# Performance work log

Hardware: AMD Instinct MI355X
Metric: run time of the kernel (lower is better)

## Reference

```python
import jax, jax.numpy as jnp
import numpy as np

T, B, IN_DIM, MEM_DIM = 512, 64, 512, 512


def _kaiming(key, shape):
    fan_in = shape[1]
    return jax.random.normal(key, shape, dtype=jnp.float32) * np.sqrt(2.0 / fan_in)


def setup_inputs() -> dict:
    key = jax.random.key(0)
    ks = jax.random.split(key, 5)
    return {
        "inputs": jax.random.normal(ks[0], (T, B, IN_DIM), dtype=jnp.float32),
        "h0": jnp.zeros((B, MEM_DIM), dtype=jnp.float32),
        "c0": jnp.zeros((B, MEM_DIM), dtype=jnp.float32),
        "W_ioux": _kaiming(ks[1], (3 * MEM_DIM, IN_DIM)),
        "b_ioux": jnp.zeros((3 * MEM_DIM,), dtype=jnp.float32),
        "W_iouh": _kaiming(ks[2], (3 * MEM_DIM, MEM_DIM)),
        "b_iouh": jnp.zeros((3 * MEM_DIM,), dtype=jnp.float32),
        "W_fx": _kaiming(ks[3], (MEM_DIM, IN_DIM)),
        "b_fx": jnp.zeros((MEM_DIM,), dtype=jnp.float32),
        "W_fh": _kaiming(ks[4], (MEM_DIM, MEM_DIM)),
        "b_fh": jnp.zeros((MEM_DIM,), dtype=jnp.float32),
    }


def reference(inputs, h0, c0, W_ioux, b_ioux, W_iouh, b_iouh, W_fx, b_fx, W_fh, b_fh):
    # Precompute input-side projections for all timesteps (one big GEMM each).
    x_iou = jnp.einsum('tbi,gi->tbg', inputs, W_ioux) + b_ioux  # [T,B,3M]
    x_f = jnp.einsum('tbi,mi->tbm', inputs, W_fx) + b_fx        # [T,B,M]

    def step(carry, xt):
        c, h = carry
        xiou_t, xf_t = xt
        iou = xiou_t + h @ W_iouh.T + b_iouh
        i, o, u = jnp.split(iou, 3, axis=-1)
        i = jax.nn.sigmoid(i)
        o = jax.nn.sigmoid(o)
        u = jnp.tanh(u)
        f = jax.nn.sigmoid(xf_t + h @ W_fh.T + b_fh)
        c_new = i * u + f * c
        h_new = o * jnp.tanh(c_new)
        return (c_new, h_new), h_new

    (c_final, h_final), output = jax.lax.scan(step, (c0, h0), (x_iou, x_f))
    # Matches torch: (stacked hidden states [T,B,M], final (c, h))
    return output, c_final, h_final
```

## Files before the change

kernel.cpp:

```cpp
#include <hip/hip_runtime.h>
#include <math.h>

#define T_STEPS 512
#define BATCH   64
#define INDIM   512
#define MEMDIM  512
#define NWG     256
#define NT      1024


#define SMEM_FLOATS (8*1028 + 4*8*68 + 16*8*68 + 2*64 + 8)

extern "C" __global__ void __launch_bounds__(NT, 1)
lstm_scan(const float* __restrict__ inputs, const float* __restrict__ h0,
          const float* __restrict__ c0,
          const float* __restrict__ W_ioux, const float* __restrict__ b_ioux,
          const float* __restrict__ W_iouh, const float* __restrict__ b_iouh,
          const float* __restrict__ W_fx,   const float* __restrict__ b_fx,
          const float* __restrict__ W_fh,   const float* __restrict__ b_fh,
          float* __restrict__ out, int* __restrict__ bar)
{
    extern __shared__ float smem[];
    float* W_s    = smem;
    float* xpart  = smem + 8*1028;
    float* hpart  = xpart + 4*8*68;
    float* c_s    = hpart + 16*8*68;
    float* bias_s = c_s + 2*64;

    float* hist = (float*)(bar + 2048);

    const int tid  = threadIdx.x;
    const int wg   = blockIdx.x;
    const int lane = tid & 63;
    const int wv16 = tid >> 6;

    const int q    = tid >> 8;
    const int r    = tid & 255;
    const int j8   = r & 7;
    const int bsub = (r >> 3) & 7;
    const int wv   = r >> 6;
    const int b0   = 16 * wv + bsub;
    const int b1   = b0 + 8;

    const int s    = lane & 31;
    const int dsub = lane >> 5;

    for (int i = tid; i < 8 * 256; i += NT) {
        int row = i >> 8;
        int c4  = i & 255;
        int mloc = row >> 2, gate = row & 3;
        int mg = 2 * wg + mloc;
        const float* src;
        if (c4 < 128) {
            const float* Wx = (gate < 3) ? (W_ioux + (size_t)(gate * 512 + mg) * INDIM)
                                         : (W_fx   + (size_t)mg * INDIM);
            src = Wx + c4 * 4;
        } else {
            const float* Wh = (gate < 3) ? (W_iouh + (size_t)(gate * 512 + mg) * MEMDIM)
                                         : (W_fh   + (size_t)mg * MEMDIM);
            src = Wh + (c4 - 128) * 4;
        }
        float4 v = *(const float4*)src;
        *(float4*)&W_s[row * 1028 + c4 * 4] = v;
    }
    if (tid < 8) {
        int mloc = tid >> 2, gate = tid & 3, mg = 2 * wg + mloc;
        bias_s[tid] = (gate < 3) ? (b_ioux[gate * 512 + mg] + b_iouh[gate * 512 + mg])
                                 : (b_fx[mg] + b_fh[mg]);
    }
    if (tid < 128) {
        int mloc = tid >> 6, b = tid & 63;
        c_s[mloc * 64 + b] = c0[(size_t)b * MEMDIM + 2 * wg + mloc];
        float hv = h0[(size_t)b * MEMDIM + 2 * wg + mloc];
        __hip_atomic_store(&hist[(2 * wg + mloc) * 64 + b], hv,
                           __ATOMIC_RELAXED, __HIP_MEMORY_SCOPE_AGENT);
    }
    __syncthreads();

    int* myflag = bar + 576 + (wg >> 4) * 32;
    if (tid == 0) {
        int n = __hip_atomic_fetch_add(&bar[(wg >> 4) * 32], 1, __ATOMIC_RELAXED,
                                       __HIP_MEMORY_SCOPE_AGENT);
        if (n == 15) {
            int m = __hip_atomic_fetch_add(&bar[512], 1, __ATOMIC_RELAXED,
                                           __HIP_MEMORY_SCOPE_AGENT);
            if (m == 15) {
                for (int l = 0; l < 16; ++l)
                    __hip_atomic_store(&bar[576 + l * 32], 1, __ATOMIC_RELAXED,
                                       __HIP_MEMORY_SCOPE_AGENT);
            }
        }
    }

    const float4* wrowx = (const float4*)&W_s[j8 * 1028] + q * 32;

    for (int t = 0; t < T_STEPS; ++t) {
        const float4* x0p = (const float4*)(inputs + ((size_t)t * BATCH + b0) * INDIM) + q * 32;
        const float4* x1p = (const float4*)(inputs + ((size_t)t * BATCH + b1) * INDIM) + q * 32;
        float4 a0 = make_float4(0.f, 0.f, 0.f, 0.f);
        float4 a1 = make_float4(0.f, 0.f, 0.f, 0.f);
#pragma unroll 8
        for (int k = 0; k < 32; ++k) {
            float4 w  = wrowx[k];
            float4 v0 = x0p[k];
            float4 v1 = x1p[k];
            a0.x += v0.x * w.x; a0.y += v0.y * w.y; a0.z += v0.z * w.z; a0.w += v0.w * w.w;
            a1.x += v1.x * w.x; a1.y += v1.y * w.y; a1.z += v1.z * w.z; a1.w += v1.w * w.w;
        }
        xpart[q * 544 + j8 * 68 + b0] = a0.x + a0.y + a0.z + a0.w;
        xpart[q * 544 + j8 * 68 + b1] = a1.x + a1.y + a1.z + a1.w;

        if (tid == 0) {
            while (__hip_atomic_load(myflag, __ATOMIC_RELAXED,
                                     __HIP_MEMORY_SCOPE_AGENT) < t + 1) {
                __builtin_amdgcn_s_sleep(1);
            }
        }
        __syncthreads();

        const unsigned long long* hrow =
            (const unsigned long long*)(hist + (size_t)(t & 1) * 32768);
        float2 hacc[8];
#pragma unroll
        for (int j = 0; j < 8; ++j) { hacc[j].x = 0.f; hacc[j].y = 0.f; }
#pragma unroll 4
        for (int it = 0; it < 16; ++it) {
            int d = wv16 * 32 + it * 2 + dsub;
            unsigned long long u = __hip_atomic_load(hrow + d * 32 + s,
                                                     __ATOMIC_RELAXED,
                                                     __HIP_MEMORY_SCOPE_AGENT);
            float2 hv = __builtin_bit_cast(float2, u);
#pragma unroll
            for (int j = 0; j < 8; ++j) {
                float wj = W_s[j * 1028 + 512 + d];
                hacc[j].x += wj * hv.x;
                hacc[j].y += wj * hv.y;
            }
        }
#pragma unroll
        for (int j = 0; j < 8; ++j) {
            hacc[j].x += __shfl_xor(hacc[j].x, 32);
            hacc[j].y += __shfl_xor(hacc[j].y, 32);
        }
        if (lane < 32) {
#pragma unroll
            for (int j = 0; j < 8; ++j)
                *(float2*)&hpart[wv16 * 544 + j * 68 + 2 * s] = hacc[j];
        }
        __syncthreads();

        float hn = 0.f, cn = 0.f;
        int mloc = tid >> 6, b = tid & 63;
        if (tid < 128) {
            float g[4];
#pragma unroll
            for (int gi = 0; gi < 4; ++gi) {
                int j = mloc * 4 + gi;
                float v = bias_s[j];
#pragma unroll
                for (int qq = 0; qq < 4; ++qq) v += xpart[qq * 544 + j * 68 + b];
#pragma unroll
                for (int w = 0; w < 16; ++w)  v += hpart[w * 544 + j * 68 + b];
                g[gi] = v;
            }
            float ig = 1.f / (1.f + expf(-g[0]));
            float og = 1.f / (1.f + expf(-g[1]));
            float ug = tanhf(g[2]);
            float fg = 1.f / (1.f + expf(-g[3]));
            cn = ig * ug + fg * c_s[mloc * 64 + b];
            c_s[mloc * 64 + b] = cn;
            hn = og * tanhf(cn);
            __hip_atomic_store(&hist[(size_t)((t + 1) & 1) * 32768
                                     + (2 * wg + mloc) * 64 + b], hn,
                               __ATOMIC_RELAXED, __HIP_MEMORY_SCOPE_AGENT);
        }
        __syncthreads();

        if (tid == 0) {
            int g16 = wg >> 4;
            int n = __hip_atomic_fetch_add(&bar[g16 * 32], 1, __ATOMIC_RELAXED,
                                           __HIP_MEMORY_SCOPE_AGENT);
            if (n == 16 * (t + 2) - 1) {
                int m = __hip_atomic_fetch_add(&bar[512], 1, __ATOMIC_RELAXED,
                                               __HIP_MEMORY_SCOPE_AGENT);
                if (m == 16 * (t + 2) - 1) {
                    for (int l = 0; l < 16; ++l)
                        __hip_atomic_store(&bar[576 + l * 32], t + 2,
                                           __ATOMIC_RELAXED, __HIP_MEMORY_SCOPE_AGENT);
                }
            }
        }

        if (tid < 128) {
            int mg = 2 * wg + mloc;
            out[((size_t)t * BATCH + b) * MEMDIM + mg] = hn;
            if (t == T_STEPS - 1) {
                out[(size_t)T_STEPS * BATCH * MEMDIM + (size_t)b * MEMDIM + mg] = cn;
                out[(size_t)T_STEPS * BATCH * MEMDIM + (size_t)BATCH * MEMDIM
                    + (size_t)b * MEMDIM + mg] = hn;
            }
        }
    }
}

extern "C" void kernel_launch(void* const* d_in, const int* in_sizes, int n_in,
                              void* d_out, int out_size, void* d_ws, size_t ws_size,
                              hipStream_t stream) {
    (void)in_sizes; (void)n_in; (void)out_size; (void)ws_size;
    const float* inputs = (const float*)d_in[0];
    const float* h0     = (const float*)d_in[1];
    const float* c0     = (const float*)d_in[2];
    const float* W_ioux = (const float*)d_in[3];
    const float* b_ioux = (const float*)d_in[4];
    const float* W_iouh = (const float*)d_in[5];
    const float* b_iouh = (const float*)d_in[6];
    const float* W_fx   = (const float*)d_in[7];
    const float* b_fx   = (const float*)d_in[8];
    const float* W_fh   = (const float*)d_in[9];
    const float* b_fh   = (const float*)d_in[10];
    float* out = (float*)d_out;
    int*   bar = (int*)d_ws;

    const size_t smem_bytes = SMEM_FLOATS * sizeof(float);
    (void)hipFuncSetAttribute((const void*)lstm_scan,
                              hipFuncAttributeMaxDynamicSharedMemorySize,
                              (int)smem_bytes);

    (void)hipMemsetAsync(d_ws, 0, 8192, stream);

    void* args[] = { (void*)&inputs, (void*)&h0, (void*)&c0,
                     (void*)&W_ioux, (void*)&b_ioux, (void*)&W_iouh, (void*)&b_iouh,
                     (void*)&W_fx, (void*)&b_fx, (void*)&W_fh, (void*)&b_fh,
                     (void*)&out, (void*)&bar };

    hipError_t err = hipLaunchCooperativeKernel((const void*)lstm_scan,
                                                dim3(NWG), dim3(NT),
                                                args, smem_bytes, stream);
    if (err != hipSuccess) {
        hipLaunchKernelGGL(lstm_scan, dim3(NWG), dim3(NT), smem_bytes, stream,
                           inputs, h0, c0, W_ioux, b_ioux, W_iouh, b_iouh,
                           W_fx, b_fx, W_fh, b_fh, out, bar);
    }
}
```

Before: 6.464 ms.

## Replace hierarchical atomic counter barrier with per-workgroup epoch flags polled by one wavefront

The grid barrier no longer uses two levels of atomic fetch-add counters plus a broadcast flag. Each workgroup now stores its step epoch into its own slot, and a 64-lane wavefront polls all 256 slots with wide loads, using a wave-wide all-vote to decide when every group has reached the step. This takes the serialized atomic RMW chain and the extra broadcast hop off the per-step critical path. In exchange, every workgroup reads all flags on each poll, which adds memory traffic. Correctness also depends on relaxed stores and loads being ordered with the h history writes.

After: 6.507 ms. No clear change (+0.7%).

```diff
diff --git a/kernel.cpp b/kernel.cpp
--- a/kernel.cpp
+++ b/kernel.cpp
@@ -77,19 +77,8 @@
     }
     __syncthreads();
 
-    int* myflag = bar + 576 + (wg >> 4) * 32;
     if (tid == 0) {
-        int n = __hip_atomic_fetch_add(&bar[(wg >> 4) * 32], 1, __ATOMIC_RELAXED,
-                                       __HIP_MEMORY_SCOPE_AGENT);
-        if (n == 15) {
-            int m = __hip_atomic_fetch_add(&bar[512], 1, __ATOMIC_RELAXED,
-                                           __HIP_MEMORY_SCOPE_AGENT);
-            if (m == 15) {
-                for (int l = 0; l < 16; ++l)
-                    __hip_atomic_store(&bar[576 + l * 32], 1, __ATOMIC_RELAXED,
-                                       __HIP_MEMORY_SCOPE_AGENT);
-            }
-        }
+        __hip_atomic_store(&bar[wg], 1, __ATOMIC_RELAXED, __HIP_MEMORY_SCOPE_AGENT);
     }
 
     const float4* wrowx = (const float4*)&W_s[j8 * 1028] + q * 32;
@@ -110,9 +99,24 @@
         xpart[q * 544 + j8 * 68 + b0] = a0.x + a0.y + a0.z + a0.w;
         xpart[q * 544 + j8 * 68 + b1] = a1.x + a1.y + a1.z + a1.w;
 
-        if (tid == 0) {
-            while (__hip_atomic_load(myflag, __ATOMIC_RELAXED,
-                                     __HIP_MEMORY_SCOPE_AGENT) < t + 1) {
+        if (tid < 64) {
+            const unsigned long long* slots = (const unsigned long long*)bar;
+            const int need = t + 1;
+            for (;;) {
+                unsigned long long v0 = __hip_atomic_load(slots + 2 * tid,
+                                                          __ATOMIC_RELAXED,
+                                                          __HIP_MEMORY_SCOPE_AGENT);
+                unsigned long long v1 = __hip_atomic_load(slots + 2 * tid + 1,
+                                                          __ATOMIC_RELAXED,
+                                                          __HIP_MEMORY_SCOPE_AGENT);
+                int e0 = (int)(unsigned)(v0 & 0xffffffffULL);
+                int e1 = (int)(unsigned)(v0 >> 32);
+                int e2 = (int)(unsigned)(v1 & 0xffffffffULL);
+                int e3 = (int)(unsigned)(v1 >> 32);
+                int m0 = e0 < e1 ? e0 : e1;
+                int m1 = e2 < e3 ? e2 : e3;
+                int mn = m0 < m1 ? m0 : m1;
+                if (__all(mn >= need)) break;
                 __builtin_amdgcn_s_sleep(1);
             }
         }
@@ -177,18 +181,8 @@
         __syncthreads();
 
         if (tid == 0) {
-            int g16 = wg >> 4;
-            int n = __hip_atomic_fetch_add(&bar[g16 * 32], 1, __ATOMIC_RELAXED,
-                                           __HIP_MEMORY_SCOPE_AGENT);
-            if (n == 16 * (t + 2) - 1) {
-                int m = __hip_atomic_fetch_add(&bar[512], 1, __ATOMIC_RELAXED,
-                                               __HIP_MEMORY_SCOPE_AGENT);
-                if (m == 16 * (t + 2) - 1) {
-                    for (int l = 0; l < 16; ++l)
-                        __hip_atomic_store(&bar[576 + l * 32], t + 2,
-                                           __ATOMIC_RELAXED, __HIP_MEMORY_SCOPE_AGENT);
-                }
-            }
+            __hip_atomic_store(&bar[wg], t + 2, __ATOMIC_RELAXED,
+                               __HIP_MEMORY_SCOPE_AGENT);
         }
 
         if (tid < 128) {
```
